# Optimization experiments

Measured on AMD Instinct MI355X. Metric: run time of the kernel, lower is better.

Reference implementation:

```python
import jax, jax.numpy as jnp
import numpy as np

H, D = 12, 768
DH = D // H  # 64

def setup_inputs() -> dict:
    key = jax.random.key(0)
    ks = jax.random.split(key, 9)
    s = 0.02
    x  = jax.random.normal(ks[0], (8, 1024, D), dtype=jnp.float32)
    Wq = jax.random.normal(ks[1], (H, D, DH), dtype=jnp.float32) * s
    Wk = jax.random.normal(ks[2], (H, D, DH), dtype=jnp.float32) * s
    Wv = jax.random.normal(ks[3], (H, D, DH), dtype=jnp.float32) * s
    bq = jax.random.normal(ks[4], (H, DH), dtype=jnp.float32) * s
    bk = jax.random.normal(ks[5], (H, DH), dtype=jnp.float32) * s
    bv = jax.random.normal(ks[6], (H, DH), dtype=jnp.float32) * s
    Wo = jax.random.normal(ks[7], (D, D), dtype=jnp.float32) * s
    bo = jax.random.normal(ks[8], (D,), dtype=jnp.float32) * s
    return {"x": x, "Wq": Wq, "Wk": Wk, "Wv": Wv, "bq": bq, "bk": bk, "bv": bv, "Wo": Wo, "bo": bo}

def reference(x, Wq, Wk, Wv, bq, bk, bv, Wo, bo):
    # x: [B,S,D]; per-head projections batched over heads: [B,H,S,DH]
    q = jnp.einsum('bsd,hde->bhse', x, Wq) + bq[None, :, None, :]
    k = jnp.einsum('bsd,hde->bhse', x, Wk) + bk[None, :, None, :]
    v = jnp.einsum('bsd,hde->bhse', x, Wv) + bv[None, :, None, :]
    scores = jnp.einsum('bhse,bhte->bhst', q, k) / jnp.sqrt(jnp.float32(DH))
    probs = jax.nn.softmax(scores, axis=-1)  # dropout is identity (p=0 / eval)
    ctx = jnp.einsum('bhst,bhte->bhse', probs, v)  # [B,H,S,DH]
    B, _, S, _ = ctx.shape
    # concat heads along feature dim (head order matches torch cat order)
    ctx = jnp.transpose(ctx, (0, 2, 1, 3)).reshape(B, S, H * DH)
    out = jnp.einsum('bsd,de->bse', ctx, Wo) + bo
    return out
```

## Files before the change

### kernel.cpp

```cpp
#include <hip/hip_runtime.h>
#include <math.h>


constexpr int NB  = 8;
constexpr int SEQ = 1024;
constexpr int NH  = 12;
constexpr int DM  = 768;
constexpr int DHD = 64;
constexpr int MROWS = NB * SEQ;
constexpr int NQKV  = 3 * NH * DHD;

typedef __attribute__((ext_vector_type(8))) short short8;
typedef __attribute__((ext_vector_type(4))) float f32x4;

#define MFMA16(a,b,c) __builtin_amdgcn_mfma_f32_16x16x32_bf16((a),(b),(c),0,0,0)

#if __has_builtin(__builtin_amdgcn_exp2f)
#define EXP2(x) __builtin_amdgcn_exp2f(x)
#else
#define EXP2(x) exp2f(x)
#endif

__device__ __forceinline__ unsigned short f2bf(float f) {
    unsigned u = __float_as_uint(f);
    return (unsigned short)((u + 0x7fffu + ((u >> 16) & 1u)) >> 16);
}
__device__ __forceinline__ unsigned short f2bf_fast(float f) {
    return (unsigned short)((__float_as_uint(f) + 0x8000u) >> 16);
}

__device__ __forceinline__ void gl_lds16(const unsigned short* g, unsigned short* l) {
    __builtin_amdgcn_global_load_lds(
        (const __attribute__((address_space(1))) void*)g,
        (__attribute__((address_space(3))) void*)l, 16, 0, 0);
}

__device__ __forceinline__ void stageK(unsigned short* lds, const unsigned short* gbase,
                                       int i, int ln, int ldg) {
    int r    = i * 8 + (ln >> 3);
    int cpos = ln & 7;
    int cdat = (cpos - r) & 7;
    gl_lds16(gbase + (size_t)r * ldg + cdat * 8, lds + i * 512);
}
__device__ __forceinline__ short8 ldK(const unsigned short* buf, int row, int chunk) {
    int c = (chunk + row) & 7;
    return *(const short8*)&buf[row * 64 + c * 8];
}

__global__ __launch_bounds__(256) void prep_k(
    const float* __restrict__ x,
    const float* __restrict__ Wq, const float* __restrict__ Wk,
    const float* __restrict__ Wv, const float* __restrict__ Wo,
    unsigned short* __restrict__ xb, unsigned short* __restrict__ wt,
    unsigned short* __restrict__ wot) {
    __shared__ float tb[64][65];
    const int blk = blockIdx.x, tid = threadIdx.x;
    if (blk < 6144) {
        const int i = blk * 256 + tid;
        float4 v = ((const float4*)x)[i];
        ushort4 o;
        o.x = f2bf(v.x); o.y = f2bf(v.y); o.z = f2bf(v.z); o.w = f2bf(v.w);
        ((ushort4*)xb)[i] = o;
        return;
    }
    const int t = blk - 6144;
    const int job = t / 144, lb = t % 144;
    const float* W;
    unsigned short* dst;
    int C, r0, c0;
    if (job < 3) {
        const float* Ws = (job == 0) ? Wq : (job == 1 ? Wk : Wv);
        const int h = lb / 12, rb = lb % 12;
        W = Ws + (size_t)h * (DM * DHD);
        dst = wt + (size_t)(job * 12 + h) * (DM * DHD);
        C = DHD; r0 = rb * 64; c0 = 0;
    } else {
        W = Wo; dst = wot; C = DM;
        r0 = (lb / 12) * 64; c0 = (lb % 12) * 64;
    }
    const int rr = tid >> 2, cc = (tid & 3) * 16;
#pragma unroll
    for (int j = 0; j < 16; j += 4) {
        float4 v = *(const float4*)&W[(size_t)(r0 + rr) * C + c0 + cc + j];
        tb[rr][cc + j + 0] = v.x;
        tb[rr][cc + j + 1] = v.y;
        tb[rr][cc + j + 2] = v.z;
        tb[rr][cc + j + 3] = v.w;
    }
    __syncthreads();
#pragma unroll
    for (int j = 0; j < 16; ++j)
        dst[(size_t)(c0 + rr) * DM + r0 + cc + j] = f2bf(tb[cc + j][rr]);
}

__global__ __launch_bounds__(256, 3) void qkv_mfma_k(
    const unsigned short* __restrict__ xb, const unsigned short* __restrict__ wt,
    const float* __restrict__ bq, const float* __restrict__ bk, const float* __restrict__ bv,
    unsigned short* __restrict__ qb, unsigned short* __restrict__ kb,
    unsigned short* __restrict__ vT) {
    __shared__ unsigned short Ah[128 * 64], Bh[128 * 64];

    const int tid = threadIdx.x;
    const int wv = tid >> 6, ln = tid & 63, quad = ln >> 4, lnid = ln & 15;
    const int wvm = wv >> 1, wvn = wv & 1;
    const int row0 = blockIdx.x * 128, col0 = blockIdx.y * 128;
    const int sel = (col0 >= 2 * DM) ? 2 : (col0 >= DM ? 1 : 0);

    f32x4 acc[4][4];
#pragma unroll
    for (int i = 0; i < 4; ++i)
#pragma unroll
        for (int j = 0; j < 4; ++j) acc[i][j] = (f32x4){0.f, 0.f, 0.f, 0.f};

    const unsigned short* Ahg = xb + (size_t)row0 * DM;
    const unsigned short* Bhg = wt + (size_t)col0 * DM;
    constexpr int NIT = DM / 64;

    if (sel < 2) {
        for (int it = 0; it < NIT; ++it) {
            const int kc = it * 64;
            __syncthreads();
#pragma unroll
            for (int c = 0; c < 4; ++c) {
                stageK(Ah, Ahg + kc, wv * 4 + c, ln, DM);
                stageK(Bh, Bhg + kc, wv * 4 + c, ln, DM);
            }
            __syncthreads();
#pragma unroll
            for (int ks = 0; ks < 2; ++ks) {
                short8 a[4], b[4];
#pragma unroll
                for (int i = 0; i < 4; ++i)
                    a[i] = ldK(Ah, wvm * 64 + i * 16 + lnid, ks * 4 + quad);
#pragma unroll
                for (int j = 0; j < 4; ++j)
                    b[j] = ldK(Bh, wvn * 64 + j * 16 + lnid, ks * 4 + quad);
#pragma unroll
                for (int j = 0; j < 4; ++j)
#pragma unroll
                    for (int i = 0; i < 4; ++i)
                        acc[j][i] = MFMA16(b[j], a[i], acc[j][i]);
            }
        }
        const float scale = (sel == 0) ? 0.18033688011112042f : 1.0f;
        const float* bias = (sel == 0) ? bq : bk;
        unsigned short* oh = (sel == 0) ? qb : kb;
#pragma unroll
        for (int et = 0; et < 4; ++et) {
            const int e = col0 + wvn * 64 + et * 16 + quad * 4;
            const int he = e - sel * DM;
            const int hh2 = he >> 6, ee = he & 63;
            float4 bs = *(const float4*)&bias[he];
#pragma unroll
            for (int st = 0; st < 4; ++st) {
                const int srow = row0 + wvm * 64 + st * 16 + lnid;
                const int bb = srow >> 10, ss = srow & (SEQ - 1);
                ushort4 pk;
                pk.x = f2bf((acc[et][st][0] + bs.x) * scale);
                pk.y = f2bf((acc[et][st][1] + bs.y) * scale);
                pk.z = f2bf((acc[et][st][2] + bs.z) * scale);
                pk.w = f2bf((acc[et][st][3] + bs.w) * scale);
                *(ushort4*)&oh[((size_t)(bb * NH + hh2) * SEQ + ss) * DHD + ee] = pk;
            }
        }
    } else {
        for (int it = 0; it < NIT; ++it) {
            const int kc = it * 64;
            __syncthreads();
#pragma unroll
            for (int c = 0; c < 4; ++c) {
                stageK(Ah, Ahg + kc, wv * 4 + c, ln, DM);
                stageK(Bh, Bhg + kc, wv * 4 + c, ln, DM);
            }
            __syncthreads();
#pragma unroll
            for (int ks = 0; ks < 2; ++ks) {
                short8 a[4], b[4];
#pragma unroll
                for (int i = 0; i < 4; ++i)
                    a[i] = ldK(Ah, wvm * 64 + i * 16 + lnid, ks * 4 + quad);
#pragma unroll
                for (int j = 0; j < 4; ++j)
                    b[j] = ldK(Bh, wvn * 64 + j * 16 + lnid, ks * 4 + quad);
#pragma unroll
                for (int i = 0; i < 4; ++i)
#pragma unroll
                    for (int j = 0; j < 4; ++j)
                        acc[i][j] = MFMA16(a[i], b[j], acc[i][j]);
            }
        }
#pragma unroll
        for (int i = 0; i < 4; ++i) {
#pragma unroll
            for (int j = 0; j < 4; ++j) {
                const int col = col0 + wvn * 64 + j * 16 + lnid;
                const int he = col - 2 * DM;
                const int hh2 = he >> 6, ee = he & 63;
                const float bs = bv[he];
                const int srow = row0 + wvm * 64 + i * 16 + quad * 4;
                const int bb = srow >> 10, ss = srow & (SEQ - 1);
                ushort4 pk;
                pk.x = f2bf(acc[i][j][0] + bs);
                pk.y = f2bf(acc[i][j][1] + bs);
                pk.z = f2bf(acc[i][j][2] + bs);
                pk.w = f2bf(acc[i][j][3] + bs);
                *(ushort4*)&vT[((size_t)(bb * NH + hh2) * DHD + ee) * SEQ + ss] = pk;
            }
        }
    }
}

__global__ __launch_bounds__(256, 3) void attn_mfma_k(
    const unsigned short* __restrict__ qb, const unsigned short* __restrict__ kb,
    const unsigned short* __restrict__ vT, unsigned short* __restrict__ ctb) {
    __shared__ unsigned short ksh[2][64 * 64], vsm[2][64 * 64];
    __shared__ unsigned short ps[128 * 72];

    const int tid = threadIdx.x;
    const int wv = tid >> 6, ln = tid & 63, quad = ln >> 4, lnid = ln & 15;
    const int bhid = blockIdx.x % 96, qt = blockIdx.x / 96;
    const int b = bhid / NH, h = bhid % NH;
    const int q0 = qt * 128;
    const unsigned short* qhb = qb + (size_t)bhid * (SEQ * DHD);
    const unsigned short* khb = kb + (size_t)bhid * (SEQ * DHD);
    const unsigned short* vTb = vT + (size_t)bhid * (DHD * SEQ);

    short8 qf[2][2];
#pragma unroll
    for (int mt = 0; mt < 2; ++mt) {
        const int srow = q0 + wv * 32 + mt * 16 + lnid;
#pragma unroll
        for (int ks_ = 0; ks_ < 2; ++ks_)
            qf[mt][ks_] = *(const short8*)(qhb + (size_t)srow * DHD + ks_ * 32 + quad * 8);
    }

    f32x4 ctx[2][4];
#pragma unroll
    for (int i = 0; i < 2; ++i)
#pragma unroll
        for (int j = 0; j < 4; ++j) ctx[i][j] = (f32x4){0.f, 0.f, 0.f, 0.f};
    float lsum[2] = {0.f, 0.f};

    stageK(ksh[0], khb, wv * 2, ln, DHD);
    stageK(ksh[0], khb, wv * 2 + 1, ln, DHD);
    stageK(vsm[0], vTb, wv * 2, ln, SEQ);
    stageK(vsm[0], vTb, wv * 2 + 1, ln, SEQ);

    for (int kt = 0; kt < SEQ / 64; ++kt) {
        const int cur = kt & 1;
        __syncthreads();
        if (kt + 1 < SEQ / 64) {
            const unsigned short* kn = khb + (kt + 1) * 64 * DHD;
            const unsigned short* vn = vTb + (kt + 1) * 64;
            stageK(ksh[cur ^ 1], kn, wv * 2, ln, DHD);
            stageK(ksh[cur ^ 1], kn, wv * 2 + 1, ln, DHD);
            stageK(vsm[cur ^ 1], vn, wv * 2, ln, SEQ);
            stageK(vsm[cur ^ 1], vn, wv * 2 + 1, ln, SEQ);
        }

        f32x4 sc[2][4];
#pragma unroll
        for (int i = 0; i < 2; ++i)
#pragma unroll
            for (int j = 0; j < 4; ++j) sc[i][j] = (f32x4){0.f, 0.f, 0.f, 0.f};
#pragma unroll
        for (int ks_ = 0; ks_ < 2; ++ks_) {
#pragma unroll
            for (int nt = 0; nt < 4; ++nt) {
                short8 k_h = ldK(ksh[cur], nt * 16 + lnid, ks_ * 4 + quad);
                sc[0][nt] = MFMA16(k_h, qf[0][ks_], sc[0][nt]);
                sc[1][nt] = MFMA16(k_h, qf[1][ks_], sc[1][nt]);
            }
        }

#pragma unroll
        for (int mt = 0; mt < 2; ++mt) {
            const int prow = wv * 32 + mt * 16 + lnid;
#pragma unroll
            for (int nt = 0; nt < 4; ++nt) {
                float p0 = EXP2(sc[mt][nt][0]);
                float p1 = EXP2(sc[mt][nt][1]);
                float p2 = EXP2(sc[mt][nt][2]);
                float p3 = EXP2(sc[mt][nt][3]);
                lsum[mt] += (p0 + p1) + (p2 + p3);
                ushort4 pw;
                pw.x = f2bf_fast(p0);
                pw.y = f2bf_fast(p1);
                pw.z = f2bf_fast(p2);
                pw.w = f2bf_fast(p3);
                *(ushort4*)&ps[prow * 72 + nt * 16 + quad * 4] = pw;
            }
        }

#pragma unroll
        for (int kvs = 0; kvs < 2; ++kvs) {
            short8 pf0 = *(const short8*)&ps[(wv * 32 + lnid) * 72 + kvs * 32 + quad * 8];
            short8 pf1 = *(const short8*)&ps[(wv * 32 + 16 + lnid) * 72 + kvs * 32 + quad * 8];
#pragma unroll
            for (int dt = 0; dt < 4; ++dt) {
                short8 vf = ldK(vsm[cur], dt * 16 + lnid, kvs * 4 + quad);
                ctx[0][dt] = MFMA16(vf, pf0, ctx[0][dt]);
                ctx[1][dt] = MFMA16(vf, pf1, ctx[1][dt]);
            }
        }
    }

#pragma unroll
    for (int mt = 0; mt < 2; ++mt) {
        float s = lsum[mt];
        s += __shfl_xor(s, 16, 64);
        s += __shfl_xor(s, 32, 64);
        const float inv = 1.0f / s;
        const int srow = b * SEQ + q0 + wv * 32 + mt * 16 + lnid;
#pragma unroll
        for (int dt = 0; dt < 4; ++dt) {
            ushort4 pk;
            pk.x = f2bf(ctx[mt][dt][0] * inv);
            pk.y = f2bf(ctx[mt][dt][1] * inv);
            pk.z = f2bf(ctx[mt][dt][2] * inv);
            pk.w = f2bf(ctx[mt][dt][3] * inv);
            *(ushort4*)&ctb[(size_t)srow * DM + h * DHD + dt * 16 + quad * 4] = pk;
        }
    }
}

__global__ __launch_bounds__(256, 3) void out_mfma_k(
    const unsigned short* __restrict__ ctb, const unsigned short* __restrict__ wot,
    const float* __restrict__ bo, float* __restrict__ out) {
    __shared__ unsigned short Ah[128 * 64], Bh[64 * 64];

    const int tid = threadIdx.x;
    const int wv = tid >> 6, ln = tid & 63, quad = ln >> 4, lnid = ln & 15;
    const int wvm = wv >> 1, wvn = wv & 1;
    const int row0 = blockIdx.x * 128, col0 = blockIdx.y * 64;

    f32x4 acc[2][4];
#pragma unroll
    for (int j = 0; j < 2; ++j)
#pragma unroll
        for (int i = 0; i < 4; ++i) acc[j][i] = (f32x4){0.f, 0.f, 0.f, 0.f};

    const unsigned short* Ahg = ctb + (size_t)row0 * DM;
    const unsigned short* Bhg = wot + (size_t)col0 * DM;

    constexpr int NIT = DM / 64;
    for (int it = 0; it < NIT; ++it) {
        const int kc = it * 64;
        __syncthreads();
#pragma unroll
        for (int c = 0; c < 4; ++c) stageK(Ah, Ahg + kc, wv * 4 + c, ln, DM);
#pragma unroll
        for (int c = 0; c < 2; ++c) stageK(Bh, Bhg + kc, wv * 2 + c, ln, DM);
        __syncthreads();
#pragma unroll
        for (int ks = 0; ks < 2; ++ks) {
            short8 a[4], b[2];
#pragma unroll
            for (int i = 0; i < 4; ++i)
                a[i] = ldK(Ah, wvm * 64 + i * 16 + lnid, ks * 4 + quad);
#pragma unroll
            for (int j = 0; j < 2; ++j)
                b[j] = ldK(Bh, wvn * 32 + j * 16 + lnid, ks * 4 + quad);
#pragma unroll
            for (int j = 0; j < 2; ++j)
#pragma unroll
                for (int i = 0; i < 4; ++i)
                    acc[j][i] = MFMA16(b[j], a[i], acc[j][i]);
        }
    }

#pragma unroll
    for (int jt = 0; jt < 2; ++jt) {
        const int colb = col0 + wvn * 32 + jt * 16 + quad * 4;
        float4 bs = *(const float4*)&bo[colb];
#pragma unroll
        for (int it = 0; it < 4; ++it) {
            const int srow = row0 + wvm * 64 + it * 16 + lnid;
            float4 o;
            o.x = acc[jt][it][0] + bs.x;
            o.y = acc[jt][it][1] + bs.y;
            o.z = acc[jt][it][2] + bs.z;
            o.w = acc[jt][it][3] + bs.w;
            *(float4*)&out[(size_t)srow * DM + colb] = o;
        }
    }
}

extern "C" void kernel_launch(void* const* d_in, const int* in_sizes, int n_in,
                              void* d_out, int out_size, void* d_ws, size_t ws_size,
                              hipStream_t stream) {
    const float* x  = (const float*)d_in[0];
    const float* Wq = (const float*)d_in[1];
    const float* Wk = (const float*)d_in[2];
    const float* Wv = (const float*)d_in[3];
    const float* bq = (const float*)d_in[4];
    const float* bk = (const float*)d_in[5];
    const float* bv = (const float*)d_in[6];
    const float* Wo = (const float*)d_in[7];
    const float* bo = (const float*)d_in[8];
    float* out = (float*)d_out;

    char* w = (char*)d_ws;
    const size_t elsX = (size_t)MROWS * DM;
    const size_t elsQ = (size_t)NB * NH * SEQ * DHD;
    unsigned short* xb  = (unsigned short*)w;
    unsigned short* ctb = xb;
    size_t off = elsX * 2;
    unsigned short* wt  = (unsigned short*)(w + off); off += (size_t)NQKV * DM * 2;
    unsigned short* wot = (unsigned short*)(w + off); off += (size_t)DM * DM * 2;
    unsigned short* qbp = (unsigned short*)(w + off); off += elsQ * 2;
    unsigned short* kbp = (unsigned short*)(w + off); off += elsQ * 2;
    unsigned short* vTp = (unsigned short*)(w + off); off += elsQ * 2;

    prep_k<<<dim3(6144 + 576), 256, 0, stream>>>(x, Wq, Wk, Wv, Wo, xb, wt, wot);
    qkv_mfma_k<<<dim3(MROWS / 128, NQKV / 128), 256, 0, stream>>>(
        xb, wt, bq, bk, bv, qbp, kbp, vTp);
    attn_mfma_k<<<dim3(768), 256, 0, stream>>>(qbp, kbp, vTp, ctb);
    out_mfma_k<<<dim3(MROWS / 128, DM / 64), 256, 0, stream>>>(ctb, wot, bo, out);
}
```

Before: 195.6 us.

## Split attention block across eight waves with swizzled P buffer in LDS

The attention kernel now runs 512 threads (8 waves) per block, and each wave handles 16 query rows instead of 32. K/V tile staging is spread over 8 waves at one stage call each. The padded P scratch buffer (stride 72) is replaced by an unpadded XOR-style swizzled layout read back through ldK, which cuts LDS use. The aim is more waves in flight to hide latency, at the cost of less K/V fragment reuse per wave and more LDS reads per MFMA.

After: 193.9 us. No clear change (-0.9%).

```diff
diff --git a/kernel.cpp b/kernel.cpp
--- a/kernel.cpp
+++ b/kernel.cpp
@@ -210,11 +210,11 @@
     }
 }
 
-__global__ __launch_bounds__(256, 3) void attn_mfma_k(
+__global__ __launch_bounds__(512, 6) void attn_mfma_k(
     const unsigned short* __restrict__ qb, const unsigned short* __restrict__ kb,
     const unsigned short* __restrict__ vT, unsigned short* __restrict__ ctb) {
     __shared__ unsigned short ksh[2][64 * 64], vsm[2][64 * 64];
-    __shared__ unsigned short ps[128 * 72];
+    __shared__ unsigned short ps[128 * 64];
 
     const int tid = threadIdx.x;
     const int wv = tid >> 6, ln = tid & 63, quad = ln >> 4, lnid = ln & 15;
@@ -225,102 +225,81 @@
     const unsigned short* khb = kb + (size_t)bhid * (SEQ * DHD);
     const unsigned short* vTb = vT + (size_t)bhid * (DHD * SEQ);
 
-    short8 qf[2][2];
-#pragma unroll
-    for (int mt = 0; mt < 2; ++mt) {
-        const int srow = q0 + wv * 32 + mt * 16 + lnid;
-#pragma unroll
-        for (int ks_ = 0; ks_ < 2; ++ks_)
-            qf[mt][ks_] = *(const short8*)(qhb + (size_t)srow * DHD + ks_ * 32 + quad * 8);
-    }
-
-    f32x4 ctx[2][4];
-#pragma unroll
-    for (int i = 0; i < 2; ++i)
-#pragma unroll
-        for (int j = 0; j < 4; ++j) ctx[i][j] = (f32x4){0.f, 0.f, 0.f, 0.f};
-    float lsum[2] = {0.f, 0.f};
-
-    stageK(ksh[0], khb, wv * 2, ln, DHD);
-    stageK(ksh[0], khb, wv * 2 + 1, ln, DHD);
-    stageK(vsm[0], vTb, wv * 2, ln, SEQ);
-    stageK(vsm[0], vTb, wv * 2 + 1, ln, SEQ);
+    const int prow = wv * 16 + lnid;
+
+    short8 qf[2];
+#pragma unroll
+    for (int ks_ = 0; ks_ < 2; ++ks_)
+        qf[ks_] = *(const short8*)(qhb + (size_t)(q0 + prow) * DHD + ks_ * 32 + quad * 8);
+
+    f32x4 ctx[4];
+#pragma unroll
+    for (int j = 0; j < 4; ++j) ctx[j] = (f32x4){0.f, 0.f, 0.f, 0.f};
+    float lsum = 0.f;
+
+    stageK(ksh[0], khb, wv, ln, DHD);
+    stageK(vsm[0], vTb, wv, ln, SEQ);
 
     for (int kt = 0; kt < SEQ / 64; ++kt) {
         const int cur = kt & 1;
         __syncthreads();
         if (kt + 1 < SEQ / 64) {
-            const unsigned short* kn = khb + (kt + 1) * 64 * DHD;
-            const unsigned short* vn = vTb + (kt + 1) * 64;
-            stageK(ksh[cur ^ 1], kn, wv * 2, ln, DHD);
-            stageK(ksh[cur ^ 1], kn, wv * 2 + 1, ln, DHD);
-            stageK(vsm[cur ^ 1], vn, wv * 2, ln, SEQ);
-            stageK(vsm[cur ^ 1], vn, wv * 2 + 1, ln, SEQ);
-        }
-
-        f32x4 sc[2][4];
-#pragma unroll
-        for (int i = 0; i < 2; ++i)
-#pragma unroll
-            for (int j = 0; j < 4; ++j) sc[i][j] = (f32x4){0.f, 0.f, 0.f, 0.f};
+            stageK(ksh[cur ^ 1], khb + (kt + 1) * 64 * DHD, wv, ln, DHD);
+            stageK(vsm[cur ^ 1], vTb + (kt + 1) * 64, wv, ln, SEQ);
+        }
+
+        f32x4 sc[4];
+#pragma unroll
+        for (int j = 0; j < 4; ++j) sc[j] = (f32x4){0.f, 0.f, 0.f, 0.f};
 #pragma unroll
         for (int ks_ = 0; ks_ < 2; ++ks_) {
 #pragma unroll
             for (int nt = 0; nt < 4; ++nt) {
-                short8 k_h = ldK(ksh[cur], nt * 16 + lnid, ks_ * 4 + quad);
-                sc[0][nt] = MFMA16(k_h, qf[0][ks_], sc[0][nt]);
-                sc[1][nt] = MFMA16(k_h, qf[1][ks_], sc[1][nt]);
-            }
-        }
-
-#pragma unroll
-        for (int mt = 0; mt < 2; ++mt) {
-            const int prow = wv * 32 + mt * 16 + lnid;
-#pragma unroll
-            for (int nt = 0; nt < 4; ++nt) {
-                float p0 = EXP2(sc[mt][nt][0]);
-                float p1 = EXP2(sc[mt][nt][1]);
-                float p2 = EXP2(sc[mt][nt][2]);
-                float p3 = EXP2(sc[mt][nt][3]);
-                lsum[mt] += (p0 + p1) + (p2 + p3);
-                ushort4 pw;
-                pw.x = f2bf_fast(p0);
-                pw.y = f2bf_fast(p1);
-                pw.z = f2bf_fast(p2);
-                pw.w = f2bf_fast(p3);
-                *(ushort4*)&ps[prow * 72 + nt * 16 + quad * 4] = pw;
-            }
+                short8 kf = ldK(ksh[cur], nt * 16 + lnid, ks_ * 4 + quad);
+                sc[nt] = MFMA16(kf, qf[ks_], sc[nt]);
+            }
+        }
+
+#pragma unroll
+        for (int nt = 0; nt < 4; ++nt) {
+            float p0 = EXP2(sc[nt][0]);
+            float p1 = EXP2(sc[nt][1]);
+            float p2 = EXP2(sc[nt][2]);
+            float p3 = EXP2(sc[nt][3]);
+            lsum += (p0 + p1) + (p2 + p3);
+            ushort4 pw;
+            pw.x = f2bf_fast(p0);
+            pw.y = f2bf_fast(p1);
+            pw.z = f2bf_fast(p2);
+            pw.w = f2bf_fast(p3);
+            const int cpos = (2 * nt + (quad >> 1) + prow) & 7;
+            *(ushort4*)&ps[prow * 64 + cpos * 8 + (quad & 1) * 4] = pw;
         }
 
 #pragma unroll
         for (int kvs = 0; kvs < 2; ++kvs) {
-            short8 pf0 = *(const short8*)&ps[(wv * 32 + lnid) * 72 + kvs * 32 + quad * 8];
-            short8 pf1 = *(const short8*)&ps[(wv * 32 + 16 + lnid) * 72 + kvs * 32 + quad * 8];
+            short8 pf = ldK(ps, prow, kvs * 4 + quad);
 #pragma unroll
             for (int dt = 0; dt < 4; ++dt) {
                 short8 vf = ldK(vsm[cur], dt * 16 + lnid, kvs * 4 + quad);
-                ctx[0][dt] = MFMA16(vf, pf0, ctx[0][dt]);
-                ctx[1][dt] = MFMA16(vf, pf1, ctx[1][dt]);
-            }
-        }
-    }
-
-#pragma unroll
-    for (int mt = 0; mt < 2; ++mt) {
-        float s = lsum[mt];
-        s += __shfl_xor(s, 16, 64);
-        s += __shfl_xor(s, 32, 64);
-        const float inv = 1.0f / s;
-        const int srow = b * SEQ + q0 + wv * 32 + mt * 16 + lnid;
-#pragma unroll
-        for (int dt = 0; dt < 4; ++dt) {
-            ushort4 pk;
-            pk.x = f2bf(ctx[mt][dt][0] * inv);
-            pk.y = f2bf(ctx[mt][dt][1] * inv);
-            pk.z = f2bf(ctx[mt][dt][2] * inv);
-            pk.w = f2bf(ctx[mt][dt][3] * inv);
-            *(ushort4*)&ctb[(size_t)srow * DM + h * DHD + dt * 16 + quad * 4] = pk;
-        }
+                ctx[dt] = MFMA16(vf, pf, ctx[dt]);
+            }
+        }
+    }
+
+    float s = lsum;
+    s += __shfl_xor(s, 16, 64);
+    s += __shfl_xor(s, 32, 64);
+    const float inv = 1.0f / s;
+    const int srow = b * SEQ + q0 + prow;
+#pragma unroll
+    for (int dt = 0; dt < 4; ++dt) {
+        ushort4 pk;
+        pk.x = f2bf(ctx[dt][0] * inv);
+        pk.y = f2bf(ctx[dt][1] * inv);
+        pk.z = f2bf(ctx[dt][2] * inv);
+        pk.w = f2bf(ctx[dt][3] * inv);
+        *(ushort4*)&ctb[(size_t)srow * DM + h * DHD + dt * 16 + quad * 4] = pk;
     }
 }
 
@@ -415,6 +394,6 @@
     prep_k<<<dim3(6144 + 576), 256, 0, stream>>>(x, Wq, Wk, Wv, Wo, xb, wt, wot);
     qkv_mfma_k<<<dim3(MROWS / 128, NQKV / 128), 256, 0, stream>>>(
         xb, wt, bq, bk, bv, qbp, kbp, vTp);
-    attn_mfma_k<<<dim3(768), 256, 0, stream>>>(qbp, kbp, vTp, ctb);
+    attn_mfma_k<<<dim3(768), 512, 0, stream>>>(qbp, kbp, vTp, ctb);
     out_mfma_k<<<dim3(MROWS / 128, DM / 64), 256, 0, stream>>>(ctb, wot, bo, out);
 }
```
